# Kernel tuning notes

Hardware: AMD Instinct MI355X
Metric: run time of the kernel (lower is better)

Reference implementation:

```python
import jax, jax.numpy as jnp
import numpy as np

# --- LCAModel hyperparameters (from init_kwargs) ---
NUM_SIMS = 2048
NUM_DIM = 8
NUM_STEPS = 1500
THRESHOLD = 1.0
LEAK = 0.1
COMPETITION = 0.1
SELF_EXC = 0.0
NOISE_STD = 1.0
DT = 0.01
SQRT_STEP = float(np.sqrt(0.001))  # hardcoded in LCALayer (sqrt(0.001), not sqrt(DT))


def setup_inputs() -> dict:
    key = jax.random.key(0)
    inp = jax.random.uniform(key, (NUM_SIMS, NUM_DIM), dtype=jnp.float32)
    return {"input": inp}


def reference(input):
    B, D = input.shape
    # gamma: off-diagonal -competition, diagonal self_excitation
    gamma = jnp.full((D, D), -COMPETITION, dtype=input.dtype)
    gamma = gamma.at[jnp.diag_indices(D)].set(SELF_EXC)
    noise_key = jax.random.key(42)

    def step(carry, t):
        pre, act = carry
        # stop integrating once any accumulator crosses threshold
        active = jnp.all(jnp.abs(act) < THRESHOLD, axis=1, keepdims=True).astype(pre.dtype)
        # faithful to torch: sum(matmul(act, gamma), dim=1, keepdim=True) -> [B, 1]
        rec = jnp.sum(act @ gamma, axis=1, keepdims=True)
        pre = pre + (input - LEAK * pre + rec) * active * DT
        dw = active * NOISE_STD * jax.random.normal(
            jax.random.fold_in(noise_key, t), (B, D), dtype=pre.dtype)
        pre = pre + dw * SQRT_STEP
        act = jax.nn.relu(pre)
        return (pre, act), (pre, act)

    init = (jnp.zeros_like(input), jnp.zeros_like(input))
    _, (pre_traj, act_traj) = jax.lax.scan(step, init, jnp.arange(NUM_STEPS))
    # prepend the zero initial state and move time to the last axis: [B, D, T+1]
    zeros = jnp.zeros((1, B, D), input.dtype)
    pre_all = jnp.moveaxis(jnp.concatenate([zeros, pre_traj], axis=0), 0, -1)
    act_all = jnp.moveaxis(jnp.concatenate([zeros, act_traj], axis=0), 0, -1)
    return (pre_all, act_all)
```

## Files before the change

### kernel.cpp

```cpp
#include <hip/hip_runtime.h>
#include <stdint.h>

#define NSIMS 2048
#define NDIM 8
#define NE (NSIMS * NDIM)
#define NSTEPS 1500
#define TP1 (NSTEPS + 1)
#define TILE 128
#define NTILE ((NSTEPS + TILE - 1) / TILE)
#define SENT 0x7fffffff

__device__ __forceinline__ void tf_block(uint32_t k0, uint32_t k1,
                                         uint32_t x0, uint32_t x1,
                                         uint32_t& o0, uint32_t& o1) {
  const uint32_t k2 = k0 ^ k1 ^ 0x1BD11BDAu;
  x0 += k0; x1 += k1;
#define TF_R(r) { x0 += x1; x1 = (x1 << (r)) | (x1 >> (32 - (r))); x1 ^= x0; }
  TF_R(13) TF_R(15) TF_R(26) TF_R(6)
  x0 += k1; x1 += k2 + 1u;
  TF_R(17) TF_R(29) TF_R(16) TF_R(24)
  x0 += k2; x1 += k0 + 2u;
  TF_R(13) TF_R(15) TF_R(26) TF_R(6)
  x0 += k0; x1 += k1 + 3u;
  TF_R(17) TF_R(29) TF_R(16) TF_R(24)
  x0 += k1; x1 += k2 + 4u;
  TF_R(13) TF_R(15) TF_R(26) TF_R(6)
  x0 += k2; x1 += k0 + 5u;
#undef TF_R
  o0 = x0; o1 = x1;
}

__device__ __forceinline__ float bits_to_normal(uint32_t bits) {
#pragma clang fp contract(off)
  const float LO = -0.99999994f;
  float f = __uint_as_float((bits >> 9) | 0x3F800000u) - 1.0f;
  float u = f * 2.0f + LO;
  u = fmaxf(LO, u);
  float t = __builtin_fmaf(-u, u, 1.0f);
  float L = __log2f(t);
  float p;
  if (L > -7.2134752f) {
    float w = __builtin_fmaf(-0.69314718f, L, -2.5f);
    p = 3.97426059e-08f;
    p = 4.85462660e-07f + p * w;
    p = -4.98282379e-06f + p * w;
    p = -6.21053119e-06f + p * w;
    p = 3.09120051e-04f + p * w;
    p = -1.77303519e-03f + p * w;
    p = -5.90813402e-03f + p * w;
    p = 3.48802730e-01f + p * w;
    p = 2.12331454e+00f + p * w;
  } else {
    float w = sqrtf(-0.69314718f * L) - 3.0f;
    p = -2.83145880e-04f;
    p = 1.42765648e-04f + p * w;
    p = 1.90826058e-03f + p * w;
    p = -5.19501312e-03f + p * w;
    p = 8.11688966e-03f + p * w;
    p = -1.07797881e-02f + p * w;
    p = 1.33485786e-02f + p * w;
    p = 1.41658104e+00f + p * w;
    p = 4.00643424e+00f + p * w;
  }
  return p * u;
}

__global__ void k_fold(uint2* __restrict__ keys) {
  int t = blockIdx.x * blockDim.x + threadIdx.x;
  if (t >= NSTEPS) return;
  uint32_t o0, o1;
  tf_block(0u, 42u, 0u, (uint32_t)t, o0, o1);
  keys[t] = make_uint2(o0, o1);
}

template <int CTRL>
__device__ __forceinline__ float dppf(float v) {
  int r = __builtin_amdgcn_update_dpp(0, __builtin_bit_cast(int, v), CTRL, 0xF, 0xF, true);
  return __builtin_bit_cast(float, r);
}
template <int CTRL>
__device__ __forceinline__ int dppi(int v) {
  return __builtin_amdgcn_update_dpp(0, v, CTRL, 0xF, 0xF, true);
}

#define STEP(ST, NZ)                                                    \
  {                                                                     \
    _Pragma("clang fp contract(off)")                                   \
    float x1 = dppf<0xB1>(act);                                         \
    float x2 = dppf<0x4E>(act);                                         \
    float x3 = dppf<0x1B>(act);                                         \
    float t1 = act + x1;                                                \
    float t2 = x2 + x3;                                                 \
    float Q = t1 + t2;                                                  \
    float S = Q + dppf<0x141>(Q);                                       \
    const float rec = (S * -0.1f) * 7.0f;   \
    float a_ = inp - 0.1f * pre;                                        \
    float b_ = a_ + rec;                                                \
    pre = pre + b_ * 0.01f;                                             \
    pre = pre + (NZ) * 0.031622776601683793f;   \
    act = fmaxf(pre, 0.0f);                                             \
    fc = (act >= 1.0f) ? (((ST) < fc) ? (ST) : fc) : fc;                \
    ptile[ST][lane] = pre;                                              \
  }

__global__ void __launch_bounds__(512) k_fused(const float* __restrict__ input,
                                               const uint2* __restrict__ keys,
                                               float* __restrict__ out) {
  __shared__ float ring[2][TILE][64];
  __shared__ float ptile[TILE][65];
  __shared__ float spre[64];
  __shared__ float sfroz[64];
  __shared__ int sfz;
  const int tid = threadIdx.x;
  const int wid = tid >> 6;
  const int lane = tid & 63;
  const int e0 = (int)blockIdx.x << 6;
  const int e = e0 + lane;
  const size_t actoff = (size_t)NE * TP1;

  if (tid == 0) sfz = SENT;

  float pre = 0.0f, act = 0.0f, inp = 0.0f, spreR = 0.0f;
  int actv = 1;
  if (wid == 0) {
    inp = input[e];
    const size_t rowo = (size_t)e * TP1;
    out[rowo] = 0.0f;
    out[actoff + rowo] = 0.0f;
  } else {
    int j = wid - 1;
    uint2 fk = keys[j];
    for (; j < TILE; j += 7) {
      const int jn = j + 7;
      uint2 fkn = (jn < TILE) ? keys[jn] : fk;
      uint32_t o0, o1;
      tf_block(fk.x, fk.y, 0u, (uint32_t)e, o0, o1);
      ring[0][j][lane] = bits_to_normal(o0 ^ o1);
      fk = fkn;
    }
  }
  __syncthreads();

  int fz = SENT;
  for (int k = 0; k < NTILE; ++k) {
    const int par = k & 1;
    const int base = k * TILE;
    const int nst = (NSTEPS - base < TILE) ? (NSTEPS - base) : TILE;
    if (wid == 0) {
      sfroz[lane] = actv ? 0.0f : 1.0f;
      spre[lane] = spreR;
      int fc = TILE;
      if (nst == TILE) {
#pragma unroll 1
        for (int ch = 0; ch < TILE / 32; ++ch) {
          float nz[32];
#pragma unroll
          for (int j = 0; j < 32; ++j) nz[j] = ring[par][ch * 32 + j][lane];
#pragma unroll
          for (int j = 0; j < 32; ++j) STEP(ch * 32 + j, nz[j])
        }
      } else {
#pragma unroll 1
        for (int ch = 0; ch < TILE / 32; ++ch) {
          float nz[32];
#pragma unroll
          for (int j = 0; j < 32; ++j) nz[j] = ring[par][ch * 32 + j][lane];
#pragma unroll
          for (int j = 0; j < 32; ++j) {
            const int st = ch * 32 + j;
            if (st >= nst) break;
            STEP(st, nz[j])
          }
        }
      }
      int c = fc;
      { int t_ = dppi<0xB1>(c);  c = (t_ < c) ? t_ : c; }
      { int t_ = dppi<0x4E>(c);  c = (t_ < c) ? t_ : c; }
      { int t_ = dppi<0x141>(c); c = (t_ < c) ? t_ : c; }
      if (actv && c < TILE) {
        const float fpre = ptile[c][lane];
        for (int s = c + 1; s < TILE; ++s) ptile[s][lane] = fpre;
        spreR = fpre;
        actv = 0;
      }
      if (__ballot(actv != 0) == 0ull) {
        spre[lane] = spreR;
        if (lane == 0) sfz = base + nst + 1;
      }
    } else {
      const int nb = base + TILE;
      int j = wid - 1;
      if (nb + j < NSTEPS) {
        uint2 fk = keys[nb + j];
        for (; j < TILE && nb + j < NSTEPS; j += 7) {
          const int tn = nb + j + 7;
          uint2 fkn = (j + 7 < TILE && tn < NSTEPS) ? keys[tn] : fk;
          uint32_t o0, o1;
          tf_block(fk.x, fk.y, 0u, (uint32_t)e, o0, o1);
          ring[par ^ 1][j][lane] = bits_to_normal(o0 ^ o1);
          fk = fkn;
        }
      }
    }
    __syncthreads();
    {
      float fm[8], sv[8];
#pragma unroll
      for (int ee = 0; ee < 8; ++ee) {
        const int el = (wid << 3) + ee;
        fm[ee] = sfroz[el];
        sv[ee] = spre[el];
      }
#pragma unroll
      for (int tb = 0; tb < TILE / 64; ++tb) {
        const int ln = nst - tb * 64;
        if (lane < ln) {
          const int tau = base + 1 + tb * 64 + lane;
#pragma unroll
          for (int ee = 0; ee < 8; ++ee) {
            const int el = (wid << 3) + ee;
            float p = ptile[tb * 64 + lane][el];
            p = (fm[ee] > 0.0f) ? sv[ee] : p;
            const size_t o = (size_t)(e0 + el) * TP1 + (size_t)tau;
            out[o] = p;
            out[actoff + o] = fmaxf(p, 0.0f);
          }
        }
      }
    }
    if (sfz != SENT) { fz = sfz; break; }
    __syncthreads();
  }

  if (fz <= NSTEPS) {
#pragma unroll
    for (int ee = 0; ee < 8; ++ee) {
      const int el = (wid << 3) + ee;
      const float p = spre[el];
      const float a = fmaxf(p, 0.0f);
      const size_t ro = (size_t)(e0 + el) * TP1;
      for (int tau = fz + lane; tau <= NSTEPS; tau += 64) {
        out[ro + (size_t)tau] = p;
        out[actoff + ro + (size_t)tau] = a;
      }
    }
  }
}

extern "C" void kernel_launch(void* const* d_in, const int* in_sizes, int n_in,
                              void* d_out, int out_size, void* d_ws, size_t ws_size,
                              hipStream_t stream) {
  const float* input = (const float*)d_in[0];
  float* out = (float*)d_out;
  uint2* keys = (uint2*)d_ws;
  if (ws_size < NSTEPS * sizeof(uint2)) return;

  k_fold<<<dim3((NSTEPS + 255) / 256), dim3(256), 0, stream>>>(keys);
  k_fused<<<dim3(NSIMS / 8), dim3(512), 0, stream>>>(input, keys, out);
}
```

Before: 134.1 us.

## Pack two dims per lane, halve tile, double elements per block

Each wave-0 lane now integrates two dimensions of a simulation (float2), so one wavefront covers 16 simulations and each block handles 128 elements. The grid drops from 256 blocks to 128, and the step tile shrinks from 128 to 64. The noise scale factor is folded into noise generation, which the seven producer waves now run with twice the work per step. The DPP reduction is shortened from four cross-lane ops to one in-lane add plus two DPP ops. The cost is fewer blocks to spread across CUs, more work per producer wave, and more tile iterations.

```diff
diff --git a/kernel.cpp b/kernel.cpp
--- a/kernel.cpp
+++ b/kernel.cpp
@@ -6,8 +6,12 @@
 #define NE (NSIMS * NDIM)
 #define NSTEPS 1500
 #define TP1 (NSTEPS + 1)
-#define TILE 128
+#define TILE 64
 #define NTILE ((NSTEPS + TILE - 1) / TILE)
+#define NBLK 128
+#define EPB 128
+#define PROW 130
+#define SQS 0.031622776601683793f
 #define SENT 0x7fffffff
 
 __device__ __forceinline__ void tf_block(uint32_t k0, uint32_t k1,
@@ -86,57 +90,62 @@
 #define STEP(ST, NZ)                                                    \
   {                                                                     \
     _Pragma("clang fp contract(off)")                                   \
-    float x1 = dppf<0xB1>(act);                                         \
-    float x2 = dppf<0x4E>(act);                                         \
-    float x3 = dppf<0x1B>(act);                                         \
-    float t1 = act + x1;                                                \
-    float t2 = x2 + x3;                                                 \
-    float Q = t1 + t2;                                                  \
-    float S = Q + dppf<0x141>(Q);                                       \
-    const float rec = (S * -0.1f) * 7.0f;   \
-    float a_ = inp - 0.1f * pre;                                        \
-    float b_ = a_ + rec;                                                \
-    pre = pre + b_ * 0.01f;                                             \
-    pre = pre + (NZ) * 0.031622776601683793f;   \
-    act = fmaxf(pre, 0.0f);                                             \
-    fc = (act >= 1.0f) ? (((ST) < fc) ? (ST) : fc) : fc;                \
-    ptile[ST][lane] = pre;                                              \
+    float h = act0 + act1;                                              \
+    float x1 = dppf<0xB1>(h);                                           \
+    float t1 = h + x1;                                                  \
+    float x2 = dppf<0x4E>(t1);                                          \
+    float S = t1 + x2;                                                  \
+    const float rec = (S * -0.1f) * 7.0f;                               \
+    float a0 = inp0 - 0.1f * pre0;                                      \
+    float a1 = inp1 - 0.1f * pre1;                                      \
+    float b0 = a0 + rec;                                                \
+    float b1 = a1 + rec;                                                \
+    pre0 = pre0 + b0 * 0.01f;                                           \
+    pre1 = pre1 + b1 * 0.01f;                                           \
+    pre0 = pre0 + (NZ).x;                                               \
+    pre1 = pre1 + (NZ).y;                                               \
+    act0 = fmaxf(pre0, 0.0f);                                           \
+    act1 = fmaxf(pre1, 0.0f);                                           \
+    float m_ = fmaxf(act0, act1);                                       \
+    fc = (m_ >= 1.0f) ? (((ST) < fc) ? (ST) : fc) : fc;                 \
+    pt2[(ST) * (PROW / 2) + lane] = make_float2(pre0, pre1);            \
   }
 
 __global__ void __launch_bounds__(512) k_fused(const float* __restrict__ input,
                                                const uint2* __restrict__ keys,
                                                float* __restrict__ out) {
-  __shared__ float ring[2][TILE][64];
-  __shared__ float ptile[TILE][65];
-  __shared__ float spre[64];
-  __shared__ float sfroz[64];
+  __shared__ float ring[2][TILE][EPB];
+  __shared__ float ptile[TILE * PROW];
+  __shared__ float spre[EPB];
+  __shared__ float sfroz[EPB];
   __shared__ int sfz;
   const int tid = threadIdx.x;
   const int wid = tid >> 6;
   const int lane = tid & 63;
-  const int e0 = (int)blockIdx.x << 6;
-  const int e = e0 + lane;
+  const int e0g = (int)blockIdx.x * EPB;
   const size_t actoff = (size_t)NE * TP1;
+  float2* const pt2 = (float2*)ptile;
+  float2* const sp2 = (float2*)spre;
+  float2* const sf2 = (float2*)sfroz;
 
   if (tid == 0) sfz = SENT;
 
-  float pre = 0.0f, act = 0.0f, inp = 0.0f, spreR = 0.0f;
+  float pre0 = 0.0f, pre1 = 0.0f, act0 = 0.0f, act1 = 0.0f;
+  float inp0 = 0.0f, inp1 = 0.0f, s0 = 0.0f, s1 = 0.0f;
   int actv = 1;
   if (wid == 0) {
-    inp = input[e];
-    const size_t rowo = (size_t)e * TP1;
-    out[rowo] = 0.0f;
-    out[actoff + rowo] = 0.0f;
+    float2 iv = ((const float2*)(input + e0g))[lane];
+    inp0 = iv.x; inp1 = iv.y;
+    const size_t r0 = (size_t)(e0g + 2 * lane) * TP1;
+    out[r0] = 0.0f;            out[actoff + r0] = 0.0f;
+    out[r0 + TP1] = 0.0f;      out[actoff + r0 + TP1] = 0.0f;
   } else {
-    int j = wid - 1;
-    uint2 fk = keys[j];
-    for (; j < TILE; j += 7) {
-      const int jn = j + 7;
-      uint2 fkn = (jn < TILE) ? keys[jn] : fk;
+    for (int rr = wid - 1; rr < 2 * TILE; rr += 7) {
+      const int st = rr >> 1, half = rr & 1;
+      const uint2 fk = keys[st];
       uint32_t o0, o1;
-      tf_block(fk.x, fk.y, 0u, (uint32_t)e, o0, o1);
-      ring[0][j][lane] = bits_to_normal(o0 ^ o1);
-      fk = fkn;
+      tf_block(fk.x, fk.y, 0u, (uint32_t)(e0g + half * 64 + lane), o0, o1);
+      ring[0][st][half * 64 + lane] = bits_to_normal(o0 ^ o1) * SQS;
     }
   }
   __syncthreads();
@@ -147,24 +156,20 @@
     const int base = k * TILE;
     const int nst = (NSTEPS - base < TILE) ? (NSTEPS - base) : TILE;
     if (wid == 0) {
-      sfroz[lane] = actv ? 0.0f : 1.0f;
-      spre[lane] = spreR;
+      const float fr = actv ? 0.0f : 1.0f;
+      sf2[lane] = make_float2(fr, fr);
+      sp2[lane] = make_float2(s0, s1);
       int fc = TILE;
-      if (nst == TILE) {
+      const float2* rg2 = (const float2*)&ring[par][0][0];
 #pragma unroll 1
-        for (int ch = 0; ch < TILE / 32; ++ch) {
-          float nz[32];
-#pragma unroll
-          for (int j = 0; j < 32; ++j) nz[j] = ring[par][ch * 32 + j][lane];
+      for (int ch = 0; ch < 2; ++ch) {
+        float2 nz[32];
+#pragma unroll
+        for (int j = 0; j < 32; ++j) nz[j] = rg2[(ch * 32 + j) * (EPB / 2) + lane];
+        if (nst == TILE) {
 #pragma unroll
           for (int j = 0; j < 32; ++j) STEP(ch * 32 + j, nz[j])
-        }
-      } else {
-#pragma unroll 1
-        for (int ch = 0; ch < TILE / 32; ++ch) {
-          float nz[32];
-#pragma unroll
-          for (int j = 0; j < 32; ++j) nz[j] = ring[par][ch * 32 + j][lane];
+        } else {
 #pragma unroll
           for (int j = 0; j < 32; ++j) {
             const int st = ch * 32 + j;
@@ -174,57 +179,51 @@
         }
       }
       int c = fc;
-      { int t_ = dppi<0xB1>(c);  c = (t_ < c) ? t_ : c; }
-      { int t_ = dppi<0x4E>(c);  c = (t_ < c) ? t_ : c; }
-      { int t_ = dppi<0x141>(c); c = (t_ < c) ? t_ : c; }
+      { int t_ = dppi<0xB1>(c); c = (t_ < c) ? t_ : c; }
+      { int t_ = dppi<0x4E>(c); c = (t_ < c) ? t_ : c; }
       if (actv && c < TILE) {
-        const float fpre = ptile[c][lane];
-        for (int s = c + 1; s < TILE; ++s) ptile[s][lane] = fpre;
-        spreR = fpre;
+        const float2 fp = pt2[c * (PROW / 2) + lane];
+        for (int s = c + 1; s < TILE; ++s) pt2[s * (PROW / 2) + lane] = fp;
+        pre0 = fp.x; pre1 = fp.y;
+        act0 = fmaxf(pre0, 0.0f); act1 = fmaxf(pre1, 0.0f);
+        s0 = pre0; s1 = pre1;
         actv = 0;
       }
       if (__ballot(actv != 0) == 0ull) {
-        spre[lane] = spreR;
+        sp2[lane] = make_float2(s0, s1);
         if (lane == 0) sfz = base + nst + 1;
       }
     } else {
       const int nb = base + TILE;
-      int j = wid - 1;
-      if (nb + j < NSTEPS) {
-        uint2 fk = keys[nb + j];
-        for (; j < TILE && nb + j < NSTEPS; j += 7) {
-          const int tn = nb + j + 7;
-          uint2 fkn = (j + 7 < TILE && tn < NSTEPS) ? keys[tn] : fk;
-          uint32_t o0, o1;
-          tf_block(fk.x, fk.y, 0u, (uint32_t)e, o0, o1);
-          ring[par ^ 1][j][lane] = bits_to_normal(o0 ^ o1);
-          fk = fkn;
-        }
+      for (int rr = wid - 1; rr < 2 * TILE; rr += 7) {
+        const int st = rr >> 1, half = rr & 1;
+        const int t = nb + st;
+        if (t >= NSTEPS) break;
+        const uint2 fk = keys[t];
+        uint32_t o0, o1;
+        tf_block(fk.x, fk.y, 0u, (uint32_t)(e0g + half * 64 + lane), o0, o1);
+        ring[par ^ 1][st][half * 64 + lane] = bits_to_normal(o0 ^ o1) * SQS;
       }
     }
     __syncthreads();
     {
-      float fm[8], sv[8];
-#pragma unroll
-      for (int ee = 0; ee < 8; ++ee) {
-        const int el = (wid << 3) + ee;
-        fm[ee] = sfroz[el];
-        sv[ee] = spre[el];
-      }
-#pragma unroll
-      for (int tb = 0; tb < TILE / 64; ++tb) {
-        const int ln = nst - tb * 64;
-        if (lane < ln) {
-          const int tau = base + 1 + tb * 64 + lane;
-#pragma unroll
-          for (int ee = 0; ee < 8; ++ee) {
-            const int el = (wid << 3) + ee;
-            float p = ptile[tb * 64 + lane][el];
-            p = (fm[ee] > 0.0f) ? sv[ee] : p;
-            const size_t o = (size_t)(e0 + el) * TP1 + (size_t)tau;
-            out[o] = p;
-            out[actoff + o] = fmaxf(p, 0.0f);
-          }
+      float fm[16], sv[16];
+#pragma unroll
+      for (int i = 0; i < 16; ++i) {
+        const int er = wid * 16 + i;
+        fm[i] = sfroz[er];
+        sv[i] = spre[er];
+      }
+      if (lane < nst) {
+        const int tau = base + 1 + lane;
+#pragma unroll
+        for (int i = 0; i < 16; ++i) {
+          const int er = wid * 16 + i;
+          float p = ptile[lane * PROW + er];
+          p = (fm[i] > 0.0f) ? sv[i] : p;
+          const size_t o = (size_t)(e0g + er) * TP1 + (size_t)tau;
+          out[o] = p;
+          out[actoff + o] = fmaxf(p, 0.0f);
         }
       }
     }
@@ -234,11 +233,11 @@
 
   if (fz <= NSTEPS) {
 #pragma unroll
-    for (int ee = 0; ee < 8; ++ee) {
-      const int el = (wid << 3) + ee;
-      const float p = spre[el];
+    for (int i = 0; i < 16; ++i) {
+      const int er = wid * 16 + i;
+      const float p = spre[er];
       const float a = fmaxf(p, 0.0f);
-      const size_t ro = (size_t)(e0 + el) * TP1;
+      const size_t ro = (size_t)(e0g + er) * TP1;
       for (int tau = fz + lane; tau <= NSTEPS; tau += 64) {
         out[ro + (size_t)tau] = p;
         out[actoff + ro + (size_t)tau] = a;
@@ -256,5 +255,5 @@
   if (ws_size < NSTEPS * sizeof(uint2)) return;
 
   k_fold<<<dim3((NSTEPS + 255) / 256), dim3(256), 0, stream>>>(keys);
-  k_fused<<<dim3(NSIMS / 8), dim3(512), 0, stream>>>(input, keys, out);
-}
+  k_fused<<<dim3(NBLK), dim3(512), 0, stream>>>(input, keys, out);
+}
```

Measured after the change: 257.1 us. 91.7% more time.
